# Kernel tuning notes

Hardware: AMD Instinct MI355X
Metric: run time of the kernel (lower is better)

## Reference

```python
import jax, jax.numpy as jnp
import numpy as np

EMBED = 1024
HEADS = 16
HEAD_DIM = EMBED // HEADS


def setup_inputs() -> dict:
    key = jax.random.key(0)
    ks = jax.random.split(key, 6)
    B, S = 4, 2048
    scale = 1.0 / np.sqrt(EMBED)
    x = jax.random.normal(ks[0], (B, S, EMBED), dtype=jnp.float32)
    Wq = jax.random.normal(ks[1], (EMBED, EMBED), dtype=jnp.float32) * scale
    Wk = jax.random.normal(ks[2], (EMBED, EMBED), dtype=jnp.float32) * scale
    Wv = jax.random.normal(ks[3], (EMBED, EMBED), dtype=jnp.float32) * scale
    Wo = jax.random.normal(ks[4], (EMBED, EMBED), dtype=jnp.float32) * scale
    bo = jnp.zeros((EMBED,), dtype=jnp.float32)
    return {"x": x, "Wq": Wq, "Wk": Wk, "Wv": Wv, "Wo": Wo, "bo": bo}


def reference(x, Wq, Wk, Wv, Wo, bo):
    B, S, E = x.shape
    H, D = HEADS, HEAD_DIM
    # nn.Linear(no bias): y = x @ W.T ; then split heads -> [B,H,S,D]
    q = (x @ Wq.T).reshape(B, S, H, D).transpose(0, 2, 1, 3)
    k = (x @ Wk.T).reshape(B, S, H, D).transpose(0, 2, 1, 3)
    v = (x @ Wv.T).reshape(B, S, H, D).transpose(0, 2, 1, 3)
    # scores [B,H,S,S] with causal mask (tril)
    energy = jnp.einsum('bhqd,bhkd->bhqk', q, k) / jnp.sqrt(jnp.float32(D))
    causal = jnp.tril(jnp.ones((S, S), dtype=bool))
    energy = jnp.where(causal[None, None], energy, jnp.float32(-jnp.inf))
    attn = jax.nn.softmax(energy, axis=-1)
    # dropout is identity in eval / p used here = 0.0
    out = jnp.einsum('bhqk,bhkd->bhqd', attn, v)
    out = out.transpose(0, 2, 1, 3).reshape(B, S, E)
    return out @ Wo.T + bo
```

## Files before the change

kernel.cpp:

```cpp
#include <hip/hip_runtime.h>
#include <math.h>

#define EMBED 1024
#define HEADS 16
#define HDIM  64
#define SEQ   2048
#define BATCH 4
#define QBLK  128
#define KVBLK 128
#define NQT   (SEQ / QBLK)
#define QSCALE 0.18033688011112042f

typedef __attribute__((ext_vector_type(8))) short short8;
typedef __attribute__((ext_vector_type(4))) float f32x4;
typedef __attribute__((ext_vector_type(16))) float f32x16;
typedef __attribute__((ext_vector_type(2))) unsigned int uint2v;

__device__ __forceinline__ unsigned short f2b(float f) {
    union { float f; unsigned int u; } c; c.f = f;
    unsigned int r = (c.u + 0x7fffu + ((c.u >> 16) & 1u)) >> 16;
    return (unsigned short)r;
}

__device__ __forceinline__ unsigned int cvtpk(float lo, float hi) {
    unsigned int r;
    asm("v_cvt_pk_bf16_f32 %0, %1, %2" : "=v"(r) : "v"(lo), "v"(hi));
    return r;
}

__device__ __forceinline__ void gld16(const void* g, void* l) {
    __builtin_amdgcn_global_load_lds((__attribute__((address_space(1))) void*)g,
                                     (__attribute__((address_space(3))) void*)l,
                                     16, 0, 0);
}

__device__ __forceinline__ f32x16 zero16() {
    f32x16 z;
#pragma unroll
    for (int i = 0; i < 16; ++i) z[i] = 0.f;
    return z;
}

__device__ __forceinline__ void makePB(const f32x16 s, short8& f0, short8& f1) {
    union { unsigned int u[4]; short8 s8; } t;
    {
        unsigned int A0 = cvtpk(s[0], s[1]), A1 = cvtpk(s[2], s[3]);
        unsigned int B0 = cvtpk(s[4], s[5]), B1 = cvtpk(s[6], s[7]);
        uint2v w0 = __builtin_amdgcn_permlane32_swap(A0, B0, false, false);
        uint2v w1 = __builtin_amdgcn_permlane32_swap(A1, B1, false, false);
        t.u[0] = w0[0]; t.u[1] = w1[0]; t.u[2] = w0[1]; t.u[3] = w1[1];
        f0 = t.s8;
    }
    {
        unsigned int A0 = cvtpk(s[8], s[9]), A1 = cvtpk(s[10], s[11]);
        unsigned int B0 = cvtpk(s[12], s[13]), B1 = cvtpk(s[14], s[15]);
        uint2v w0 = __builtin_amdgcn_permlane32_swap(A0, B0, false, false);
        uint2v w1 = __builtin_amdgcn_permlane32_swap(A1, B1, false, false);
        t.u[0] = w0[0]; t.u[1] = w1[0]; t.u[2] = w0[1]; t.u[3] = w1[1];
        f1 = t.s8;
    }
}

__global__ __launch_bounds__(256) void cast_bf16(const float* __restrict__ src,
                                                 unsigned short* __restrict__ dst,
                                                 int n) {
    int i = (blockIdx.x * 256 + threadIdx.x) * 8;
    if (i >= n) return;
    float4 a = *(const float4*)(src + i);
    float4 b = *(const float4*)(src + i + 4);
    short8 v;
    v[0] = (short)f2b(a.x); v[1] = (short)f2b(a.y);
    v[2] = (short)f2b(a.z); v[3] = (short)f2b(a.w);
    v[4] = (short)f2b(b.x); v[5] = (short)f2b(b.y);
    v[6] = (short)f2b(b.z); v[7] = (short)f2b(b.w);
    *(short8*)(dst + i) = v;
}

template <int MODE>
__global__ __launch_bounds__(256) void gemm_bf16(const unsigned short* __restrict__ A,
                                                 const unsigned short* __restrict__ W,
                                                 void* __restrict__ outp,
                                                 const float* __restrict__ bias) {
    const int K_ = EMBED;
    __shared__ __attribute__((aligned(16))) unsigned short As[128 * 32];
    __shared__ __attribute__((aligned(16))) unsigned short Bs[128 * 32];

    const int tid  = threadIdx.x;
    const int lane = tid & 63;
    const int w    = tid >> 6;
    const int wr   = w >> 1, wc = w & 1;
    const int m0 = blockIdx.y * 128, n0 = blockIdx.x * 128;

    const unsigned short* gA = A + (size_t)(m0 + w * 32 + (lane >> 2)) * K_ + (lane & 3) * 8;
    const unsigned short* gB = W + (size_t)(n0 + w * 32 + (lane >> 2)) * K_ + (lane & 3) * 8;
    unsigned short* lA = As + (w * 32) * 32;
    unsigned short* lB = Bs + (w * 32) * 32;

    f32x4 zero = {0.f, 0.f, 0.f, 0.f};
    f32x4 acc[4][4];
#pragma unroll
    for (int i = 0; i < 4; ++i)
#pragma unroll
        for (int j = 0; j < 4; ++j) acc[i][j] = zero;

    for (int k0 = 0; k0 < K_; k0 += 32) {
        gld16(gA, lA);
        gld16(gA + (size_t)16 * K_, lA + 16 * 32);
        gld16(gB, lB);
        gld16(gB + (size_t)16 * K_, lB + 16 * 32);
        gA += 32; gB += 32;
        __syncthreads();
        short8 af[4], bfr[4];
#pragma unroll
        for (int i = 0; i < 4; ++i) {
            af[i]  = *(const short8*)&As[(wr * 64 + i * 16 + (lane & 15)) * 32 + (lane >> 4) * 8];
            bfr[i] = *(const short8*)&Bs[(wc * 64 + i * 16 + (lane & 15)) * 32 + (lane >> 4) * 8];
        }
#pragma unroll
        for (int i = 0; i < 4; ++i)
#pragma unroll
            for (int j = 0; j < 4; ++j)
                acc[i][j] = __builtin_amdgcn_mfma_f32_16x16x32_bf16(af[i], bfr[j], acc[i][j], 0, 0, 0);
        __syncthreads();
    }

    if (MODE == 0) {
        const size_t PP = (size_t)BATCH * SEQ * EMBED;
        unsigned short* dst = (unsigned short*)outp;
#pragma unroll
        for (int i = 0; i < 4; ++i)
#pragma unroll
            for (int ni = 0; ni < 4; ++ni) {
                int n = n0 + wc * 64 + ni * 16 + (lane & 15);
                int which = n >> 10;
                int h = (n >> 6) & 15, d = n & 63;
                float os = (which == 0) ? QSCALE : 1.0f;
#pragma unroll
                for (int j = 0; j < 4; ++j) {
                    int m = m0 + wr * 64 + i * 16 + (lane >> 4) * 4 + j;
                    int b = m >> 11, s = m & (SEQ - 1);
                    dst[(size_t)which * PP + (((size_t)b * HEADS + h) * SEQ + s) * HDIM + d] =
                        f2b(acc[i][ni][j] * os);
                }
            }
    } else {
        float* dst = (float*)outp;
#pragma unroll
        for (int i = 0; i < 4; ++i)
#pragma unroll
            for (int ni = 0; ni < 4; ++ni) {
                int n = n0 + wc * 64 + ni * 16 + (lane & 15);
                float bv = bias[n];
#pragma unroll
                for (int j = 0; j < 4; ++j) {
                    int m = m0 + wr * 64 + i * 16 + (lane >> 4) * 4 + j;
                    dst[(size_t)m * EMBED + n] = acc[i][ni][j] + bv;
                }
            }
    }
}

__global__ __launch_bounds__(256, 2) void attn_mfma32(const unsigned short* __restrict__ Q,
                                                      const unsigned short* __restrict__ K,
                                                      const unsigned short* __restrict__ V,
                                                      unsigned short* __restrict__ att) {
    __shared__ __attribute__((aligned(16))) unsigned short KsL[2][KVBLK * 64];
    __shared__ __attribute__((aligned(16))) unsigned short VtL[2][64 * KVBLK];

    const int tid  = threadIdx.x;
    const int lane = tid & 63;
    const int wv   = tid >> 6;
    const int hi   = lane >> 5;
    const int lq   = lane & 31;
    const int bh   = blockIdx.y;
    const int qtA  = (NQT - 1) - blockIdx.x;
    const int qtB  = blockIdx.x;
    const size_t base = (size_t)bh * SEQ * HDIM;

    const int krow = tid >> 3;
    const int kxor = ((tid & 7) ^ (krow & 7)) * 8;
    const int vkp = tid & 63, vo = (tid >> 6) * 2;

    const int ksw = (lq & 7) << 4;

    short8 qf[4];
    auto loadQ = [&](int qt) {
        const unsigned short* qrow =
            Q + base + (size_t)(qt * QBLK + wv * 32 + lq) * HDIM + hi * 8;
        qf[0] = *(const short8*)(qrow);
        qf[1] = *(const short8*)(qrow + 16);
        qf[2] = *(const short8*)(qrow + 32);
        qf[3] = *(const short8*)(qrow + 48);
    };

    auto stageK = [&](int k0, int bufi) {
        const unsigned short* g0 = K + base + (size_t)(k0 + krow) * HDIM + kxor;
        unsigned short* l0 = &KsL[bufi][wv * 512];
#pragma unroll
        for (int j = 0; j < 4; ++j)
            gld16(g0 + (size_t)(32 * j) * HDIM, l0 + j * 2048);
    };

    short8 va0, vb0, va1, vb1;
    auto loadV = [&](int k0) {
        const unsigned short* vp = V + base + (size_t)(k0 + 2 * vkp) * HDIM;
        va0 = *(const short8*)(vp + vo * 8);
        vb0 = *(const short8*)(vp + HDIM + vo * 8);
        va1 = *(const short8*)(vp + (vo + 1) * 8);
        vb1 = *(const short8*)(vp + HDIM + (vo + 1) * 8);
    };
    auto writeV = [&](int bufi) {
        char* vb_ = (char*)&VtL[bufi][0];
#pragma unroll
        for (int e = 0; e < 8; ++e) {
            unsigned int p0 = (unsigned int)(unsigned short)va0[e] |
                              ((unsigned int)(unsigned short)vb0[e] << 16);
            *(unsigned int*)(vb_ + ((vo * 8 + e) << 8) + ((4 * vkp) ^ (e << 4))) = p0;
            unsigned int p1 = (unsigned int)(unsigned short)va1[e] |
                              ((unsigned int)(unsigned short)vb1[e] << 16);
            *(unsigned int*)(vb_ + (((vo + 1) * 8 + e) << 8) + ((4 * vkp) ^ (e << 4))) = p1;
        }
    };

    f32x16 o0 = zero16(), o1 = zero16();
    float m_run = -INFINITY, l_run = 0.f;

    const int b_ = bh >> 4, h_ = bh & 15;
    auto writeOut = [&](int q0w_) {
        const float invl = 1.f / l_run;
        unsigned short* orow =
            att + ((size_t)b_ * SEQ + (q0w_ + lq)) * EMBED + h_ * HDIM + 4 * hi;
#pragma unroll
        for (int c = 0; c < 4; ++c) {
            unsigned int w0 = cvtpk(o0[4 * c] * invl, o0[4 * c + 1] * invl);
            unsigned int w1 = cvtpk(o0[4 * c + 2] * invl, o0[4 * c + 3] * invl);
            *(uint2*)(orow + 8 * c) = make_uint2(w0, w1);
            unsigned int w2 = cvtpk(o1[4 * c] * invl, o1[4 * c + 1] * invl);
            unsigned int w3 = cvtpk(o1[4 * c + 2] * invl, o1[4 * c + 3] * invl);
            *(uint2*)(orow + 32 + 8 * c) = make_uint2(w2, w3);
        }
    };

    loadQ(qtA);
    int qtCur = qtA;
    int q0w = qtA * QBLK + wv * 32;
    int qsel = q0w + lq;
    stageK(0, 0);
    loadV(0);
    writeV(0);
    __syncthreads();

    const int niter = NQT + 1;
    for (int i = 0; i < niter; ++i) {
        const int buf = i & 1, nbuf = buf ^ 1;
        const int kt = (i <= qtA) ? i : (i - qtA - 1);
        const int k0 = kt * KVBLK;
        const bool pf = (i + 1 < niter);

        if (pf) {
            const int ktN = (i + 1 <= qtA) ? (i + 1) : (i - qtA);
            const int k0N = ktN * KVBLK;
            stageK(k0N, nbuf);
            loadV(k0N);
        }

        const char* kbase = (const char*)&KsL[buf][0];
        f32x16 sS[4];
        __builtin_amdgcn_s_setprio(1);
#pragma unroll
        for (int c = 0; c < 4; ++c) {
            const char* kb_ = kbase + ((c * 32 + lq) << 7);
            f32x16 acc = zero16();
#pragma unroll
            for (int dc = 0; dc < 4; ++dc) {
                short8 kf = *(const short8*)(kb_ + ((((dc << 1) | hi) << 4) ^ ksw));
                acc = __builtin_amdgcn_mfma_f32_32x32x16_bf16(kf, qf[dc], acc, 0, 0, 0);
            }
            sS[c] = acc;
        }
        __builtin_amdgcn_s_setprio(0);

        if (kt == qtCur) {
#pragma unroll
            for (int c = 0; c < 4; ++c)
#pragma unroll
                for (int r = 0; r < 16; ++r) {
                    int key = k0 + 32 * c + (r & 3) + 8 * (r >> 2) + 4 * hi;
                    if (key > qsel) sS[c][r] = -INFINITY;
                }
        }

        f32x16 t;
#pragma unroll
        for (int r = 0; r < 16; ++r)
            t[r] = fmaxf(fmaxf(sS[0][r], sS[1][r]), fmaxf(sS[2][r], sS[3][r]));
        float m8[8];
#pragma unroll
        for (int r = 0; r < 8; ++r) m8[r] = fmaxf(t[r], t[r + 8]);
        float m4[4];
#pragma unroll
        for (int r = 0; r < 4; ++r) m4[r] = fmaxf(m8[r], m8[r + 4]);
        float mx = fmaxf(fmaxf(m4[0], m4[1]), fmaxf(m4[2], m4[3]));
        mx = fmaxf(mx, __shfl_xor(mx, 32));

        if (__any(mx > m_run + 8.0f)) {
            float mnew = fmaxf(m_run, mx);
            float scl = __builtin_exp2f(m_run - mnew);
            m_run = mnew;
            l_run *= scl;
#pragma unroll
            for (int r = 0; r < 16; ++r) { o0[r] *= scl; o1[r] *= scl; }
        }

#pragma unroll
        for (int c = 0; c < 4; ++c)
#pragma unroll
            for (int r = 0; r < 16; ++r)
                sS[c][r] = __builtin_exp2f(sS[c][r] - m_run);

        f32x16 u;
#pragma unroll
        for (int r = 0; r < 16; ++r)
            u[r] = (sS[0][r] + sS[1][r]) + (sS[2][r] + sS[3][r]);
        float s8[8];
#pragma unroll
        for (int r = 0; r < 8; ++r) s8[r] = u[r] + u[r + 8];
        float s4[4];
#pragma unroll
        for (int r = 0; r < 4; ++r) s4[r] = s8[r] + s8[r + 4];
        float ps = (s4[0] + s4[1]) + (s4[2] + s4[3]);
        ps += __shfl_xor(ps, 32);
        l_run += ps;

        const char* vtb = (const char*)&VtL[buf][0];
        __builtin_amdgcn_s_setprio(1);
#pragma unroll
        for (int c = 0; c < 4; ++c) {
            short8 pb0, pb1;
            makePB(sS[c], pb0, pb1);
            short8 vf;
            vf = *(const short8*)(vtb + (lq << 8) + ((c * 64 + hi * 16) ^ ksw));
            o0 = __builtin_amdgcn_mfma_f32_32x32x16_bf16(vf, pb0, o0, 0, 0, 0);
            vf = *(const short8*)(vtb + (lq << 8) + ((c * 64 + 32 + hi * 16) ^ ksw));
            o0 = __builtin_amdgcn_mfma_f32_32x32x16_bf16(vf, pb1, o0, 0, 0, 0);
            vf = *(const short8*)(vtb + ((32 + lq) << 8) + ((c * 64 + hi * 16) ^ ksw));
            o1 = __builtin_amdgcn_mfma_f32_32x32x16_bf16(vf, pb0, o1, 0, 0, 0);
            vf = *(const short8*)(vtb + ((32 + lq) << 8) + ((c * 64 + 32 + hi * 16) ^ ksw));
            o1 = __builtin_amdgcn_mfma_f32_32x32x16_bf16(vf, pb1, o1, 0, 0, 0);
        }
        __builtin_amdgcn_s_setprio(0);

        if (pf) writeV(nbuf);
        __syncthreads();

        if (i == qtA) {
            writeOut(q0w);
            o0 = zero16(); o1 = zero16();
            m_run = -INFINITY; l_run = 0.f;
            loadQ(qtB);
            qtCur = qtB;
            q0w = qtB * QBLK + wv * 32;
            qsel = q0w + lq;
        }
    }
    writeOut(q0w);
}

extern "C" void kernel_launch(void* const* d_in, const int* in_sizes, int n_in,
                              void* d_out, int out_size, void* d_ws, size_t ws_size,
                              hipStream_t stream) {
    const float* x  = (const float*)d_in[0];
    const float* Wq = (const float*)d_in[1];
    const float* Wk = (const float*)d_in[2];
    const float* Wv = (const float*)d_in[3];
    const float* Wo = (const float*)d_in[4];
    const float* bo = (const float*)d_in[5];

    const size_t XN = (size_t)BATCH * SEQ * EMBED;
    const size_t WN = (size_t)EMBED * EMBED;

    unsigned short* ws   = (unsigned short*)d_ws;
    unsigned short* xb   = ws;
    unsigned short* wqkv = xb + XN;
    unsigned short* wob  = wqkv + 3 * WN;
    unsigned short* Qb   = wob + WN;
    unsigned short* attb = Qb + 3 * XN;

    cast_bf16<<<(int)(XN / 2048), 256, 0, stream>>>(x, xb, (int)XN);
    cast_bf16<<<(int)(WN / 2048), 256, 0, stream>>>(Wq, wqkv, (int)WN);
    cast_bf16<<<(int)(WN / 2048), 256, 0, stream>>>(Wk, wqkv + WN, (int)WN);
    cast_bf16<<<(int)(WN / 2048), 256, 0, stream>>>(Wv, wqkv + 2 * WN, (int)WN);
    cast_bf16<<<(int)(WN / 2048), 256, 0, stream>>>(Wo, wob, (int)WN);

    gemm_bf16<0><<<dim3(3 * EMBED / 128, BATCH * SEQ / 128), 256, 0, stream>>>(
        xb, wqkv, Qb, nullptr);

    attn_mfma32<<<dim3(NQT / 2, BATCH * HEADS), 256, 0, stream>>>(
        Qb, Qb + XN, Qb + 2 * XN, attb);

    gemm_bf16<1><<<dim3(EMBED / 128, BATCH * SEQ / 128), 256, 0, stream>>>(
        attb, wob, d_out, bo);
}
```

Before: 194.9 us.

## Skip fully masked key halves on diagonal tile and merge cast kernels

Splits each 128-key attention tile into two 64-key halves, each with its own softmax and PV step. The second half is skipped when every key in it lies past the wave's last query row, which removes fully masked QK and PV MFMA work on the diagonal tile. The five fp32-to-bf16 cast launches are also merged into one kernel that picks its source by block index, saving launch overhead. In exchange, the online softmax now does two max/rescale passes per tile instead of one, adding some VALU and shuffle work on every tile.

```diff
diff --git a/kernel.cpp b/kernel.cpp
--- a/kernel.cpp
+++ b/kernel.cpp
@@ -61,18 +61,32 @@
     }
 }
 
-__global__ __launch_bounds__(256) void cast_bf16(const float* __restrict__ src,
-                                                 unsigned short* __restrict__ dst,
-                                                 int n) {
-    int i = (blockIdx.x * 256 + threadIdx.x) * 8;
-    if (i >= n) return;
+__global__ __launch_bounds__(256) void cast_all(const float* __restrict__ x,
+                                                const float* __restrict__ wq,
+                                                const float* __restrict__ wk,
+                                                const float* __restrict__ wv,
+                                                const float* __restrict__ wo,
+                                                unsigned short* __restrict__ xb,
+                                                unsigned short* __restrict__ wqkv,
+                                                unsigned short* __restrict__ wob) {
+    const int WNblk = 512;
+    int b = blockIdx.x;
+    const float* src;
+    unsigned short* dst;
+    int off;
+    if (b < 4096)            { src = x;  dst = xb;                    off = b; }
+    else if (b < 4096 + WNblk)   { src = wq; dst = wqkv;              off = b - 4096; }
+    else if (b < 4096 + 2*WNblk) { src = wk; dst = wqkv + 1024*1024;  off = b - 4096 - WNblk; }
+    else if (b < 4096 + 3*WNblk) { src = wv; dst = wqkv + 2*1024*1024; off = b - 4096 - 2*WNblk; }
+    else                     { src = wo; dst = wob;                   off = b - 4096 - 3*WNblk; }
+    int i = (off * 256 + threadIdx.x) * 8;
     float4 a = *(const float4*)(src + i);
-    float4 b = *(const float4*)(src + i + 4);
+    float4 c = *(const float4*)(src + i + 4);
     short8 v;
     v[0] = (short)f2b(a.x); v[1] = (short)f2b(a.y);
     v[2] = (short)f2b(a.z); v[3] = (short)f2b(a.w);
-    v[4] = (short)f2b(b.x); v[5] = (short)f2b(b.y);
-    v[6] = (short)f2b(b.z); v[7] = (short)f2b(b.w);
+    v[4] = (short)f2b(c.x); v[5] = (short)f2b(c.y);
+    v[6] = (short)f2b(c.z); v[7] = (short)f2b(c.w);
     *(short8*)(dst + i) = v;
 }
 
@@ -180,7 +194,6 @@
     const int krow = tid >> 3;
     const int kxor = ((tid & 7) ^ (krow & 7)) * 8;
     const int vkp = tid & 63, vo = (tid >> 6) * 2;
-
     const int ksw = (lq & 7) << 4;
 
     short8 qf[4];
@@ -259,96 +272,111 @@
 
         if (pf) {
             const int ktN = (i + 1 <= qtA) ? (i + 1) : (i - qtA);
-            const int k0N = ktN * KVBLK;
-            stageK(k0N, nbuf);
-            loadV(k0N);
+            stageK(ktN * KVBLK, nbuf);
+            loadV(ktN * KVBLK);
         }
 
         const char* kbase = (const char*)&KsL[buf][0];
-        f32x16 sS[4];
+        const char* vtb   = (const char*)&VtL[buf][0];
+        const bool diag = (kt == qtCur);
+        const bool doH1 = (k0 + 64 <= q0w + 31);
+
+        f32x16 sA0 = zero16(), sB0 = zero16(), sA1, sB1;
         __builtin_amdgcn_s_setprio(1);
 #pragma unroll
-        for (int c = 0; c < 4; ++c) {
-            const char* kb_ = kbase + ((c * 32 + lq) << 7);
-            f32x16 acc = zero16();
+        for (int dc = 0; dc < 4; ++dc) {
+            const int kofs = ((((dc << 1) | hi) << 4) ^ ksw);
+            short8 kf0 = *(const short8*)(kbase + ((0 * 32 + lq) << 7) + kofs);
+            short8 kf1 = *(const short8*)(kbase + ((1 * 32 + lq) << 7) + kofs);
+            sA0 = __builtin_amdgcn_mfma_f32_32x32x16_bf16(kf0, qf[dc], sA0, 0, 0, 0);
+            sB0 = __builtin_amdgcn_mfma_f32_32x32x16_bf16(kf1, qf[dc], sB0, 0, 0, 0);
+        }
+        if (doH1) {
+            sA1 = zero16(); sB1 = zero16();
 #pragma unroll
             for (int dc = 0; dc < 4; ++dc) {
-                short8 kf = *(const short8*)(kb_ + ((((dc << 1) | hi) << 4) ^ ksw));
-                acc = __builtin_amdgcn_mfma_f32_32x32x16_bf16(kf, qf[dc], acc, 0, 0, 0);
-            }
-            sS[c] = acc;
+                const int kofs = ((((dc << 1) | hi) << 4) ^ ksw);
+                short8 kf2 = *(const short8*)(kbase + ((2 * 32 + lq) << 7) + kofs);
+                short8 kf3 = *(const short8*)(kbase + ((3 * 32 + lq) << 7) + kofs);
+                sA1 = __builtin_amdgcn_mfma_f32_32x32x16_bf16(kf2, qf[dc], sA1, 0, 0, 0);
+                sB1 = __builtin_amdgcn_mfma_f32_32x32x16_bf16(kf3, qf[dc], sB1, 0, 0, 0);
+            }
         }
         __builtin_amdgcn_s_setprio(0);
 
-        if (kt == qtCur) {
-#pragma unroll
-            for (int c = 0; c < 4; ++c)
+        auto smaxPV = [&](f32x16& sA, f32x16& sB, int key0, int cA) {
+            if (diag) {
 #pragma unroll
                 for (int r = 0; r < 16; ++r) {
-                    int key = k0 + 32 * c + (r & 3) + 8 * (r >> 2) + 4 * hi;
-                    if (key > qsel) sS[c][r] = -INFINITY;
+                    int key = key0 + (r & 3) + 8 * (r >> 2) + 4 * hi;
+                    if (key > qsel) sA[r] = -INFINITY;
+                    if (key + 32 > qsel) sB[r] = -INFINITY;
                 }
-        }
-
-        f32x16 t;
-#pragma unroll
-        for (int r = 0; r < 16; ++r)
-            t[r] = fmaxf(fmaxf(sS[0][r], sS[1][r]), fmaxf(sS[2][r], sS[3][r]));
-        float m8[8];
-#pragma unroll
-        for (int r = 0; r < 8; ++r) m8[r] = fmaxf(t[r], t[r + 8]);
-        float m4[4];
-#pragma unroll
-        for (int r = 0; r < 4; ++r) m4[r] = fmaxf(m8[r], m8[r + 4]);
-        float mx = fmaxf(fmaxf(m4[0], m4[1]), fmaxf(m4[2], m4[3]));
-        mx = fmaxf(mx, __shfl_xor(mx, 32));
-
-        if (__any(mx > m_run + 8.0f)) {
-            float mnew = fmaxf(m_run, mx);
-            float scl = __builtin_exp2f(m_run - mnew);
-            m_run = mnew;
-            l_run *= scl;
-#pragma unroll
-            for (int r = 0; r < 16; ++r) { o0[r] *= scl; o1[r] *= scl; }
-        }
-
-#pragma unroll
-        for (int c = 0; c < 4; ++c)
-#pragma unroll
-            for (int r = 0; r < 16; ++r)
-                sS[c][r] = __builtin_exp2f(sS[c][r] - m_run);
-
-        f32x16 u;
-#pragma unroll
-        for (int r = 0; r < 16; ++r)
-            u[r] = (sS[0][r] + sS[1][r]) + (sS[2][r] + sS[3][r]);
-        float s8[8];
-#pragma unroll
-        for (int r = 0; r < 8; ++r) s8[r] = u[r] + u[r + 8];
-        float s4[4];
-#pragma unroll
-        for (int r = 0; r < 4; ++r) s4[r] = s8[r] + s8[r + 4];
-        float ps = (s4[0] + s4[1]) + (s4[2] + s4[3]);
-        ps += __shfl_xor(ps, 32);
-        l_run += ps;
-
-        const char* vtb = (const char*)&VtL[buf][0];
-        __builtin_amdgcn_s_setprio(1);
-#pragma unroll
-        for (int c = 0; c < 4; ++c) {
-            short8 pb0, pb1;
-            makePB(sS[c], pb0, pb1);
+            }
+            f32x16 t;
+#pragma unroll
+            for (int r = 0; r < 16; ++r) t[r] = fmaxf(sA[r], sB[r]);
+            float m8[8];
+#pragma unroll
+            for (int r = 0; r < 8; ++r) m8[r] = fmaxf(t[r], t[r + 8]);
+            float m4[4];
+#pragma unroll
+            for (int r = 0; r < 4; ++r) m4[r] = fmaxf(m8[r], m8[r + 4]);
+            float mx = fmaxf(fmaxf(m4[0], m4[1]), fmaxf(m4[2], m4[3]));
+            mx = fmaxf(mx, __shfl_xor(mx, 32));
+
+            if (__any(mx > m_run + 8.0f)) {
+                float mnew = fmaxf(m_run, mx);
+                float scl = __builtin_exp2f(m_run - mnew);
+                m_run = mnew;
+                l_run *= scl;
+#pragma unroll
+                for (int r = 0; r < 16; ++r) { o0[r] *= scl; o1[r] *= scl; }
+            }
+#pragma unroll
+            for (int r = 0; r < 16; ++r) {
+                sA[r] = __builtin_exp2f(sA[r] - m_run);
+                sB[r] = __builtin_exp2f(sB[r] - m_run);
+            }
+            f32x16 u;
+#pragma unroll
+            for (int r = 0; r < 16; ++r) u[r] = sA[r] + sB[r];
+            float s8[8];
+#pragma unroll
+            for (int r = 0; r < 8; ++r) s8[r] = u[r] + u[r + 8];
+            float s4[4];
+#pragma unroll
+            for (int r = 0; r < 4; ++r) s4[r] = s8[r] + s8[r + 4];
+            float ps = (s4[0] + s4[1]) + (s4[2] + s4[3]);
+            ps += __shfl_xor(ps, 32);
+            l_run += ps;
+
+            short8 pA0, pA1, pB0, pB1;
+            makePB(sA, pA0, pA1);
+            makePB(sB, pB0, pB1);
+            __builtin_amdgcn_s_setprio(1);
             short8 vf;
-            vf = *(const short8*)(vtb + (lq << 8) + ((c * 64 + hi * 16) ^ ksw));
-            o0 = __builtin_amdgcn_mfma_f32_32x32x16_bf16(vf, pb0, o0, 0, 0, 0);
-            vf = *(const short8*)(vtb + (lq << 8) + ((c * 64 + 32 + hi * 16) ^ ksw));
-            o0 = __builtin_amdgcn_mfma_f32_32x32x16_bf16(vf, pb1, o0, 0, 0, 0);
-            vf = *(const short8*)(vtb + ((32 + lq) << 8) + ((c * 64 + hi * 16) ^ ksw));
-            o1 = __builtin_amdgcn_mfma_f32_32x32x16_bf16(vf, pb0, o1, 0, 0, 0);
-            vf = *(const short8*)(vtb + ((32 + lq) << 8) + ((c * 64 + 32 + hi * 16) ^ ksw));
-            o1 = __builtin_amdgcn_mfma_f32_32x32x16_bf16(vf, pb1, o1, 0, 0, 0);
-        }
-        __builtin_amdgcn_s_setprio(0);
+            vf = *(const short8*)(vtb + (lq << 8) + ((cA * 64 + hi * 16) ^ ksw));
+            o0 = __builtin_amdgcn_mfma_f32_32x32x16_bf16(vf, pA0, o0, 0, 0, 0);
+            vf = *(const short8*)(vtb + (lq << 8) + ((cA * 64 + 32 + hi * 16) ^ ksw));
+            o0 = __builtin_amdgcn_mfma_f32_32x32x16_bf16(vf, pA1, o0, 0, 0, 0);
+            vf = *(const short8*)(vtb + ((32 + lq) << 8) + ((cA * 64 + hi * 16) ^ ksw));
+            o1 = __builtin_amdgcn_mfma_f32_32x32x16_bf16(vf, pA0, o1, 0, 0, 0);
+            vf = *(const short8*)(vtb + ((32 + lq) << 8) + ((cA * 64 + 32 + hi * 16) ^ ksw));
+            o1 = __builtin_amdgcn_mfma_f32_32x32x16_bf16(vf, pA1, o1, 0, 0, 0);
+            vf = *(const short8*)(vtb + (lq << 8) + (((cA + 1) * 64 + hi * 16) ^ ksw));
+            o0 = __builtin_amdgcn_mfma_f32_32x32x16_bf16(vf, pB0, o0, 0, 0, 0);
+            vf = *(const short8*)(vtb + (lq << 8) + (((cA + 1) * 64 + 32 + hi * 16) ^ ksw));
+            o0 = __builtin_amdgcn_mfma_f32_32x32x16_bf16(vf, pB1, o0, 0, 0, 0);
+            vf = *(const short8*)(vtb + ((32 + lq) << 8) + (((cA + 1) * 64 + hi * 16) ^ ksw));
+            o1 = __builtin_amdgcn_mfma_f32_32x32x16_bf16(vf, pB0, o1, 0, 0, 0);
+            vf = *(const short8*)(vtb + ((32 + lq) << 8) + (((cA + 1) * 64 + 32 + hi * 16) ^ ksw));
+            o1 = __builtin_amdgcn_mfma_f32_32x32x16_bf16(vf, pB1, o1, 0, 0, 0);
+            __builtin_amdgcn_s_setprio(0);
+        };
+
+        smaxPV(sA0, sB0, k0, 0);
+        if (doH1) smaxPV(sA1, sB1, k0 + 64, 2);
 
         if (pf) writeV(nbuf);
         __syncthreads();
@@ -386,11 +414,7 @@
     unsigned short* Qb   = wob + WN;
     unsigned short* attb = Qb + 3 * XN;
 
-    cast_bf16<<<(int)(XN / 2048), 256, 0, stream>>>(x, xb, (int)XN);
-    cast_bf16<<<(int)(WN / 2048), 256, 0, stream>>>(Wq, wqkv, (int)WN);
-    cast_bf16<<<(int)(WN / 2048), 256, 0, stream>>>(Wk, wqkv + WN, (int)WN);
-    cast_bf16<<<(int)(WN / 2048), 256, 0, stream>>>(Wv, wqkv + 2 * WN, (int)WN);
-    cast_bf16<<<(int)(WN / 2048), 256, 0, stream>>>(Wo, wob, (int)WN);
+    cast_all<<<4096 + 4 * 512, 256, 0, stream>>>(x, Wq, Wk, Wv, Wo, xb, wqkv, wob);
 
     gemm_bf16<0><<<dim3(3 * EMBED / 128, BATCH * SEQ / 128), 256, 0, stream>>>(
         xb, wqkv, Qb, nullptr);
```

Result: no change. 195.7 us (+0.4%).

## Fuse cast launches and remap block indices to be XCD-aware

Applied to the files above, without the earlier changes.

The five separate bf16 cast launches become a single kernel that picks its source and destination from the block index. Both GEMMs and the attention kernel now use a 1D grid and remap block IDs so that consecutive blocks on the same XCD (bid&7) cover contiguous tiles or heads. The intent is to cut launch overhead and improve L2 locality across the MI355X's chiplets. The hard-coded block counts tie the code to the fixed problem sizes.

```diff
diff --git a/kernel.cpp b/kernel.cpp
--- a/kernel.cpp
+++ b/kernel.cpp
@@ -61,18 +61,32 @@
     }
 }
 
-__global__ __launch_bounds__(256) void cast_bf16(const float* __restrict__ src,
-                                                 unsigned short* __restrict__ dst,
-                                                 int n) {
-    int i = (blockIdx.x * 256 + threadIdx.x) * 8;
-    if (i >= n) return;
+__global__ __launch_bounds__(256) void cast_all(const float* __restrict__ x,
+                                                const float* __restrict__ wq,
+                                                const float* __restrict__ wk,
+                                                const float* __restrict__ wv,
+                                                const float* __restrict__ wo,
+                                                unsigned short* __restrict__ xb,
+                                                unsigned short* __restrict__ wqkv,
+                                                unsigned short* __restrict__ wob) {
+    const int WNblk = 512;
+    int b = blockIdx.x;
+    const float* src;
+    unsigned short* dst;
+    int off;
+    if (b < 4096)            { src = x;  dst = xb;                    off = b; }
+    else if (b < 4096 + WNblk)   { src = wq; dst = wqkv;              off = b - 4096; }
+    else if (b < 4096 + 2*WNblk) { src = wk; dst = wqkv + 1024*1024;  off = b - 4096 - WNblk; }
+    else if (b < 4096 + 3*WNblk) { src = wv; dst = wqkv + 2*1024*1024; off = b - 4096 - 2*WNblk; }
+    else                     { src = wo; dst = wob;                   off = b - 4096 - 3*WNblk; }
+    int i = (off * 256 + threadIdx.x) * 8;
     float4 a = *(const float4*)(src + i);
-    float4 b = *(const float4*)(src + i + 4);
+    float4 c = *(const float4*)(src + i + 4);
     short8 v;
     v[0] = (short)f2b(a.x); v[1] = (short)f2b(a.y);
     v[2] = (short)f2b(a.z); v[3] = (short)f2b(a.w);
-    v[4] = (short)f2b(b.x); v[5] = (short)f2b(b.y);
-    v[6] = (short)f2b(b.z); v[7] = (short)f2b(b.w);
+    v[4] = (short)f2b(c.x); v[5] = (short)f2b(c.y);
+    v[6] = (short)f2b(c.z); v[7] = (short)f2b(c.w);
     *(short8*)(dst + i) = v;
 }
 
@@ -89,7 +103,11 @@
     const int lane = tid & 63;
     const int w    = tid >> 6;
     const int wr   = w >> 1, wc = w & 1;
-    const int m0 = blockIdx.y * 128, n0 = blockIdx.x * 128;
+
+    const int nbx = (MODE == 0) ? 24 : 8;
+    const int cpx = (MODE == 0) ? 192 : 64;
+    const int nb  = (blockIdx.x & 7) * cpx + (blockIdx.x >> 3);
+    const int m0 = (nb / nbx) * 128, n0 = (nb % nbx) * 128;
 
     const unsigned short* gA = A + (size_t)(m0 + w * 32 + (lane >> 2)) * K_ + (lane & 3) * 8;
     const unsigned short* gB = W + (size_t)(n0 + w * 32 + (lane >> 2)) * K_ + (lane & 3) * 8;
@@ -172,15 +190,16 @@
     const int wv   = tid >> 6;
     const int hi   = lane >> 5;
     const int lq   = lane & 31;
-    const int bh   = blockIdx.y;
-    const int qtA  = (NQT - 1) - blockIdx.x;
-    const int qtB  = blockIdx.x;
+    const int bid  = blockIdx.x;
+    const int pair = bid >> 6;
+    const int bh   = (bid & 7) * 8 + ((bid >> 3) & 7);
+    const int qtA  = (NQT - 1) - pair;
+    const int qtB  = pair;
     const size_t base = (size_t)bh * SEQ * HDIM;
 
     const int krow = tid >> 3;
     const int kxor = ((tid & 7) ^ (krow & 7)) * 8;
     const int vkp = tid & 63, vo = (tid >> 6) * 2;
-
     const int ksw = (lq & 7) << 4;
 
     short8 qf[4];
@@ -259,9 +278,8 @@
 
         if (pf) {
             const int ktN = (i + 1 <= qtA) ? (i + 1) : (i - qtA);
-            const int k0N = ktN * KVBLK;
-            stageK(k0N, nbuf);
-            loadV(k0N);
+            stageK(ktN * KVBLK, nbuf);
+            loadV(ktN * KVBLK);
         }
 
         const char* kbase = (const char*)&KsL[buf][0];
@@ -386,18 +404,12 @@
     unsigned short* Qb   = wob + WN;
     unsigned short* attb = Qb + 3 * XN;
 
-    cast_bf16<<<(int)(XN / 2048), 256, 0, stream>>>(x, xb, (int)XN);
-    cast_bf16<<<(int)(WN / 2048), 256, 0, stream>>>(Wq, wqkv, (int)WN);
-    cast_bf16<<<(int)(WN / 2048), 256, 0, stream>>>(Wk, wqkv + WN, (int)WN);
-    cast_bf16<<<(int)(WN / 2048), 256, 0, stream>>>(Wv, wqkv + 2 * WN, (int)WN);
-    cast_bf16<<<(int)(WN / 2048), 256, 0, stream>>>(Wo, wob, (int)WN);
-
-    gemm_bf16<0><<<dim3(3 * EMBED / 128, BATCH * SEQ / 128), 256, 0, stream>>>(
-        xb, wqkv, Qb, nullptr);
-
-    attn_mfma32<<<dim3(NQT / 2, BATCH * HEADS), 256, 0, stream>>>(
+    cast_all<<<4096 + 4 * 512, 256, 0, stream>>>(x, Wq, Wk, Wv, Wo, xb, wqkv, wob);
+
+    gemm_bf16<0><<<1536, 256, 0, stream>>>(xb, wqkv, Qb, nullptr);
+
+    attn_mfma32<<<(NQT / 2) * BATCH * HEADS, 256, 0, stream>>>(
         Qb, Qb + XN, Qb + 2 * XN, attb);
 
-    gemm_bf16<1><<<dim3(EMBED / 128, BATCH * SEQ / 128), 256, 0, stream>>>(
-        attb, wob, d_out, bo);
-}
+    gemm_bf16<1><<<512, 256, 0, stream>>>(attb, wob, d_out, bo);
+}
```

New measurement: 179.2 us. 1.09x faster.
